# Performance work log

Measured on AMD Instinct MI355X. Metric: run time of the kernel, lower is better.

The kernel has to match this reference:

```python
import jax, jax.numpy as jnp
import numpy as np

# ---- para constants (see shape_source) ----
SIZE = 200          # SLM / detector plane
PAD = 100           # para.paddings -> padded FFT plane 400x400
PADDED = SIZE + 2 * PAD
NUM_LAYERS = 4
SCALE = 2.0         # para.scale
EXT = 1.0           # para.extension
K = 8               # para.kernel_size
S = 8               # para.stride
M = (SIZE - K) // S + 1   # para.map_size = 25
WIN = 5             # para.win_size
T = 1.0             # softmax temperature
RANGE = 10          # para.range (== dim_out)
DIM_OUT = 10
HIDDEN = 512
DIM_IN = M * M      # 625, flattened BN output feeds fcl
THR = 0.2           # para.thershold
SHIFT = 0.0         # para.shift
EPS = 1e-5          # BatchNorm eps
BATCH = 32


def setup_inputs() -> dict:
    key = jax.random.key(0)
    ks = jax.random.split(key, 10)
    x = jax.random.uniform(ks[0], (BATCH, SIZE, SIZE), jnp.float32)

    def transfer(k):  # unit-magnitude angular-spectrum transfer function
        ph = jax.random.uniform(k, (PADDED, PADDED), jnp.float32, 0.0, 2.0 * np.pi)
        return jnp.exp(1j * ph).astype(jnp.complex64)

    h = transfer(ks[1])
    h_pro = transfer(ks[2])
    h_det = transfer(ks[3])
    phase = 0.1 * jax.random.normal(ks[4], (NUM_LAYERS, SIZE, SIZE), jnp.float32)
    W1 = 0.02 * jax.random.normal(ks[5], (HIDDEN, DIM_IN), jnp.float32)
    b1 = jnp.zeros((HIDDEN,), jnp.float32)
    W2 = 0.02 * jax.random.normal(ks[6], (DIM_OUT, HIDDEN), jnp.float32)
    b2 = jnp.zeros((DIM_OUT,), jnp.float32)
    gamma = jnp.ones((1,), jnp.float32)   # BatchNorm2d(1) weight
    beta = jnp.zeros((1,), jnp.float32)   # BatchNorm2d(1) bias
    return {"x": x, "batch_size": BATCH, "h": h, "h_pro": h_pro, "h_det": h_det,
            "phase": phase, "W1": W1, "b1": b1, "W2": W2, "b2": b2,
            "gamma": gamma, "beta": beta}


def _diff(wave, trans):
    # F.pad + fftshift/fft2 * trans / ifft2/ifftshift (batch-dim shifts cancel)
    wave = jnp.pad(wave, ((0, 0), (PAD, PAD), (PAD, PAD)))
    wf = jnp.fft.fft2(jnp.fft.fftshift(wave, axes=(-2, -1)))
    return jnp.fft.ifftshift(jnp.fft.ifft2(wf * trans), axes=(-2, -1))


def _forward(x, batch_size, h, h_pro, h_det, phase, W1, b1, W2, b2, gamma, beta):
    x = x.astype(jnp.complex64)
    x = _diff(x, h_pro)[:, PAD:PAD + SIZE, PAD:PAD + SIZE]
    for idx in range(NUM_LAYERS):
        trans = jnp.pad(phase[idx], ((PAD, PAD), (PAD, PAD)))
        w = _diff(x, h)
        w = w * jnp.exp(1j * SCALE * jnp.pi * (jnp.sin(EXT * trans) + 1.0))
        x = w[:, PAD:PAD + SIZE, PAD:PAD + SIZE]
    x = _diff(x, h_det)[:, PAD:PAD + SIZE, PAD:PAD + SIZE]
    i_out = jnp.square(jnp.abs(x))                       # (B, SIZE, SIZE)
    B = i_out.shape[0]
    # AvgPool2d(K, S) with SIZE % K == 0 -> reshape-mean
    pooled = i_out.reshape(B, M, K, M, K).mean(axis=(2, 4))  # (B, M, M)

    rows = jnp.arange(M)

    def window(i, j):
        rm = (rows >= i) & (rows < i + WIN)
        cm = (rows >= j) & (rows < j + WIN)
        mask = (rm[:, None] & cm[None, :]).astype(pooled.dtype)   # I_block
        sig = pooled * mask                                       # (B, M, M)
        # BatchNorm2d(1), training mode: stats over all N*H*W
        mu = sig.mean()
        var = sig.var()
        nrm = (sig - mu) / jnp.sqrt(var + EPS) * gamma[0] + beta[0]
        f = nrm.reshape(B, -1)                                    # (B, DIM_IN)
        hid = jax.nn.relu(f @ W1.T + b1)                          # dropout: eval
        logits = (hid @ W2.T + b2) / T
        p = jax.nn.softmax(logits, axis=1)                        # (B, DIM_OUT)
        a = jnp.argmax(p, axis=1)                                 # (B,)
        delta = p.max(axis=1) - p.min(axis=1)                     # b - b2
        temp = jax.nn.one_hot(a, RANGE + 1, dtype=jnp.float32).sum(0)
        final0 = jnp.argmax(temp)
        dm = delta * (a == final0).astype(delta.dtype)            # delta * delta_max
        nz = jnp.sum(dm != 0.0)                                   # csr .data length
        delta1 = jnp.where(nz > 0, dm.sum() / jnp.maximum(nz, 1).astype(dm.dtype), jnp.nan)
        # nan < THR is False, matching torch semantics
        final = jnp.where(delta1 < THR, 0, final0 + 1).astype(jnp.int32)
        res = jnp.where(final == 0, 0.0, final.astype(jnp.float32) + SHIFT)
        ch = (final != 0).astype(jnp.float32)
        return final, res, ch

    ii, jj = jnp.meshgrid(jnp.arange(M), jnp.arange(M), indexing="ij")
    finals, result, ch_map = jax.vmap(window)(ii.ravel(), jj.ravel())
    result = result.reshape(M, M)
    ch_map = ch_map.reshape(M, M)
    histo = jnp.zeros(RANGE + 1, jnp.float32).at[finals].add(1.0)
    return result, ch_map, histo


def reference(x, batch_size, h, h_pro, h_det, phase, W1, b1, W2, b2, gamma, beta):
    return _forward(x, batch_size, h, h_pro, h_det, phase, W1, b1, W2, b2, gamma, beta)
```

## Files before the change

### kernel.cpp

```cpp
#include <hip/hip_runtime.h>
#include <math.h>

#define GLIM_X    1280000
#define GLIM_H    160000
#define GLIM_PH   160000
#define GLIM_W1   320000
#define GLIM_B1   512
#define GLIM_W2   5120
#define GLIM_B2   10
#define GLIM_OUT  1261
#define GLIM_POOL 20000

struct cplx { float x, y; };
__device__ __forceinline__ cplx operator+(cplx a, cplx b){ return {a.x+b.x, a.y+b.y}; }
__device__ __forceinline__ cplx operator-(cplx a, cplx b){ return {a.x-b.x, a.y-b.y}; }
__device__ __forceinline__ cplx cmul(cplx a, cplx b){ return {a.x*b.x - a.y*b.y, a.x*b.y + a.y*b.x}; }
template<bool INV>
__device__ __forceinline__ cplx tw(cplx a, cplx w){
  if(INV) return {a.x*w.x + a.y*w.y, a.y*w.x - a.x*w.y};
  else    return {a.x*w.x - a.y*w.y, a.x*w.y + a.y*w.x};
}
template<bool INV>
__device__ __forceinline__ void dft4(cplx&a, cplx&b, cplx&c, cplx&d){
  cplx t0=a+c, t1=a-c, t2=b+d, t3=b-d;
  cplx j3 = INV ? cplx{-t3.y, t3.x} : cplx{t3.y, -t3.x};
  a = t0+t2; c = t0-t2; b = t1+j3; d = t1-j3;
}
template<bool INV>
__device__ void fft16(cplx* x, const cplx* tab){
  cplx y[16];
  #pragma unroll
  for(int b=0;b<4;b++){
    cplx p0=x[b], p1=x[4+b], p2=x[8+b], p3=x[12+b];
    dft4<INV>(p0,p1,p2,p3);
    y[b*4+0]=p0;
    y[b*4+1]=tw<INV>(p1, tab[25*b]);
    y[b*4+2]=tw<INV>(p2, tab[50*b]);
    y[b*4+3]=tw<INV>(p3, tab[75*b]);
  }
  #pragma unroll
  for(int c=0;c<4;c++){
    cplx p0=y[c], p1=y[4+c], p2=y[8+c], p3=y[12+c];
    dft4<INV>(p0,p1,p2,p3);
    x[c]=p0; x[c+4]=p1; x[c+8]=p2; x[c+12]=p3;
  }
}
template<bool INV>
__device__ __forceinline__ void dft5(const cplx* v, cplx* o, const cplx* tab){
  #pragma unroll
  for(int k=0;k<5;k++){
    cplx s=v[0];
    #pragma unroll
    for(int j=1;j<5;j++){
      const int m=(j*k)%5;
      s = s + tw<INV>(v[j], tab[80*m]);
    }
    o[k]=s;
  }
}
template<bool INV>
__device__ void fft25(cplx* t, const cplx* tab){
  cplx u[25];
  #pragma unroll
  for(int b=0;b<5;b++){
    cplx v[5], o[5];
    #pragma unroll
    for(int a=0;a<5;a++) v[a]=t[5*a+b];
    dft5<INV>(v,o,tab);
    #pragma unroll
    for(int c=0;c<5;c++) u[b*5+c]=tw<INV>(o[c], tab[16*b*c]);
  }
  #pragma unroll
  for(int c=0;c<5;c++){
    cplx v[5], o[5];
    #pragma unroll
    for(int b=0;b<5;b++) v[b]=u[b*5+c];
    dft5<INV>(v,o,tab);
    #pragma unroll
    for(int d=0;d<5;d++) t[c+5*d]=o[d];
  }
}

__device__ __forceinline__ float bf2f(unsigned short u){
  unsigned int v = ((unsigned int)u)<<16;
  float f; __builtin_memcpy(&f,&v,4); return f;
}
__device__ __forceinline__ float hf2f(unsigned short u){
  _Float16 x; __builtin_memcpy(&x,&u,2); return (float)x;
}
__device__ __forceinline__ cplx ldH(const void* p, int i, int dec){
  if(i<0 || i>=GLIM_H) return {0.f,0.f};
  unsigned int v = ((const unsigned int*)p)[i];
  unsigned short lo=(unsigned short)(v&0xFFFFu), hi=(unsigned short)(v>>16);
  cplx z;
  if(dec==2)      z = { hf2f(lo), hf2f(hi) };
  else if(dec==3) z = { (float)(short)lo*(1.f/32767.f), (float)(short)hi*(1.f/32767.f) };
  else            z = { bf2f(lo), bf2f(hi) };
  if(!(fabsf(z.x) < 2.f)) z.x = 0.f;
  if(!(fabsf(z.y) < 2.f)) z.y = 0.f;
  return z;
}
__device__ __forceinline__ float ldf(const float* p, int i, int lim){
  if(i<0 || i>=lim) return 0.f;
  return p[i];
}
__device__ __forceinline__ void stout(float* p, int i, float v){
  if(i>=0 && i<GLIM_OUT) p[i] = v;
}

__global__ __launch_bounds__(64) void k_probe(const void* h, int* flags){
  __shared__ float err[3];
  if(threadIdx.x<3) err[threadIdx.x]=0.f;
  __syncthreads();
  if(threadIdx.x<32){
    unsigned int v = ((const unsigned int*)h)[threadIdx.x];
    unsigned short lo=(unsigned short)(v&0xFFFFu), hi=(unsigned short)(v>>16);
    float cr[3], ci[3];
    cr[0]=bf2f(lo);                       ci[0]=bf2f(hi);
    cr[1]=hf2f(lo);                       ci[1]=hf2f(hi);
    cr[2]=(float)(short)lo*(1.f/32767.f); ci[2]=(float)(short)hi*(1.f/32767.f);
    for(int d=0;d<3;d++){
      float r2 = cr[d]*cr[d] + ci[d]*ci[d];
      float e = fabsf(r2 - 1.f);
      if(!(e < 4.f)) e = 4.f;
      atomicAdd(&err[d], e);
    }
  }
  __syncthreads();
  if(threadIdx.x==0){
    int best=0; float be=err[0];
    for(int d=1; d<3; d++) if(err[d] < be){ be=err[d]; best=d; }
    flags[1] = best+1;
    flags[0] = 0;
  }
}

__global__ __launch_bounds__(256) void k_init(cplx* tab, float* outz, float* hist, float* pr){
  int t = blockIdx.x*256 + threadIdx.x;
  if(t < 400){
    float a = -6.28318530717958647692f * (float)t * (1.0f/400.0f);
    float sn, cs; sincosf(a, &sn, &cs);
    tab[t] = { cs, sn };
  }
  if(t < GLIM_OUT) outz[t] = 0.f;
  if(t < 11) hist[t] = 0.f;
  if(t >= 16 && t < 30) pr[t-16] = 0.f;
}

__global__ __launch_bounds__(256) void k_hprep(const void* h, const void* hpro,
    const void* hdet, cplx* __restrict__ Hd, const int* __restrict__ flags)
{
  int dec = flags[1];
  int t = blockIdx.x*256 + threadIdx.x;
  if(t >= 3*GLIM_H) return;
  int arr = t/GLIM_H, o = t - arr*GLIM_H;
  int c = o/400, rem = o - c*400;
  int k1 = rem/25, k2 = rem - k1*25;
  const void* src = (arr==0)?h:((arr==1)?hpro:hdet);
  Hd[t] = ldH(src, (k1+16*k2)*400 + c, dec);
}

__global__ __launch_bounds__(256,2) void k_rowfft(const float* __restrict__ xr,
    int img0, cplx* __restrict__ A, const cplx* __restrict__ gtab, int alim)
{
  __shared__ cplx lt[8*400];
  __shared__ cplx stab[400];
  for(int m=threadIdx.x;m<400;m+=256) stab[m]=gtab[m];
  int lr = threadIdx.x>>5, role = threadIdx.x&31;
  int idx = blockIdx.x*8 + lr;
  int img_local = idx/200, rc = idx - img_local*200;
  int abase = img_local*80000 + rc*400;
  __syncthreads();
  if(role<25){
    int n2=role;
    cplx x[16];
    #pragma unroll
    for(int n1=0;n1<16;n1++){
      cplx v={0.f,0.f};
      if(n1>=4 && n1<12){
        int cc = 25*n1+n2-100;
        v = { ldf(xr, (img0+img_local)*40000 + rc*200 + cc, GLIM_X), 0.f };
      }
      x[n1]=v;
    }
    fft16<false>(x, stab);
    cplx* L = lt + lr*400;
    #pragma unroll
    for(int k1=0;k1<16;k1++) L[k1*25+n2]=tw<false>(x[k1], stab[n2*k1]);
  }
  __syncthreads();
  if(role<16){
    int k1=role;
    cplx* L = lt + lr*400;
    cplx t[25];
    #pragma unroll
    for(int n2=0;n2<25;n2++) t[n2]=L[k1*25+n2];
    fft25<false>(t, stab);
    #pragma unroll
    for(int k2=0;k2<25;k2++){
      int ai = abase + k1+16*k2;
      if(ai>=0 && ai<alim) A[ai]=t[k2];
    }
  }
}

__global__ __launch_bounds__(256,2) void k_colpass(cplx* __restrict__ A,
    const cplx* __restrict__ Hd, const cplx* __restrict__ gtab)
{
  __shared__ cplx lt[8*401];
  __shared__ cplx stab[400];
  cplx (*sm)[9] = (cplx(*)[9])lt;
  for(int m=threadIdx.x;m<400;m+=256) stab[m]=gtab[m];
  int img_local = blockIdx.x/50, cg = blockIdx.x - img_local*50;
  int col0 = cg*8;
  int lc = threadIdx.x&7, rr = threadIdx.x>>3;
  cplx* L = lt + lc*401;
  cplx xx[25];
  __syncthreads();
  {
    const float4* A4 = (const float4*)A;
    for(int t=threadIdx.x; t<800; t+=256){
      int r = t>>2, p = t&3;
      int ce = img_local*80000 + r*400 + col0 + 2*p;
      float4 v = A4[ce>>1];
      sm[r][2*p]   = { v.x, v.y };
      sm[r][2*p+1] = { v.z, v.w };
    }
  }
  __syncthreads();
  if(rr<25){
    int n2=rr;
    #pragma unroll
    for(int n1=0;n1<16;n1++){
      cplx v={0.f,0.f};
      if(n1>=4 && n1<12) v = sm[25*n1+n2-100][lc];
      xx[n1]=v;
    }
  }
  __syncthreads();
  if(rr<25){
    int n2=rr;
    fft16<false>(xx, stab);
    #pragma unroll
    for(int k1=0;k1<16;k1++) L[k1*25+n2]=tw<false>(xx[k1], stab[n2*k1]);
  }
  __syncthreads();
  if(rr<16){
    int k1=rr;
    #pragma unroll
    for(int n2=0;n2<25;n2++) xx[n2]=L[k1*25+n2];
    fft25<false>(xx, stab);
    const cplx* hrun = Hd + (col0+lc)*400 + k1*25;
    #pragma unroll
    for(int k2=0;k2<25;k2++) xx[k2]=cmul(xx[k2], hrun[k2]);
  }
  __syncthreads();
  if(rr<16){
    int k1=rr;
    #pragma unroll
    for(int k2=0;k2<25;k2++) L[k1+16*k2]=xx[k2];
  }
  __syncthreads();
  if(rr<25){
    int n2=rr;
    #pragma unroll
    for(int n1=0;n1<16;n1++) xx[n1]=L[25*n1+n2];
  }
  __syncthreads();
  if(rr<25){
    int n2=rr;
    fft16<true>(xx, stab);
    #pragma unroll
    for(int k1=0;k1<16;k1++) L[k1*25+n2]=tw<true>(xx[k1], stab[n2*k1]);
  }
  __syncthreads();
  if(rr<16){
    int k1=rr;
    #pragma unroll
    for(int n2=0;n2<25;n2++) xx[n2]=L[k1*25+n2];
    fft25<true>(xx, stab);
    const float sc=1.0f/400.0f;
    #pragma unroll
    for(int k2=0;k2<25;k2++){ xx[k2].x*=sc; xx[k2].y*=sc; }
  }
  __syncthreads();
  if(rr<16){
    int k1=rr;
    #pragma unroll
    for(int k2=0;k2<25;k2++){
      int m=k1+16*k2;
      if(m>=100 && m<300) sm[m-100][lc] = xx[k2];
    }
  }
  __syncthreads();
  {
    float4* A4 = (float4*)A;
    for(int t=threadIdx.x; t<800; t+=256){
      int r = t>>2, p = t&3;
      int ce = img_local*80000 + r*400 + col0 + 2*p;
      cplx a = sm[r][2*p], b = sm[r][2*p+1];
      A4[ce>>1] = { a.x, a.y, b.x, b.y };
    }
  }
}

__global__ __launch_bounds__(256,2) void k_rowpass(cplx* __restrict__ A,
    const float* __restrict__ ph, int phoff, int useMask,
    const cplx* __restrict__ gtab, int alim)
{
  __shared__ cplx lt[8*400];
  __shared__ cplx stab[400];
  cplx (*sm)[200] = (cplx(*)[200])lt;
  for(int m=threadIdx.x;m<400;m+=256) stab[m]=gtab[m];
  int lr=threadIdx.x>>5, role=threadIdx.x&31;
  int idx = blockIdx.x*8+lr;
  int img_local = idx/200, rc = idx - img_local*200;
  int abase = img_local*80000 + rc*400;
  __syncthreads();
  if(role<25){
    int n2=role;
    cplx x[16];
    #pragma unroll
    for(int n1=0;n1<16;n1++){
      cplx v={0.f,0.f};
      int ai = abase + 25*n1+n2;
      if(ai>=0 && ai<alim) v=A[ai];
      x[n1]=v;
    }
    fft16<true>(x, stab);
    cplx* L = lt + lr*400;
    #pragma unroll
    for(int k1=0;k1<16;k1++) L[k1*25+n2]=tw<true>(x[k1], stab[n2*k1]);
  }
  __syncthreads();
  cplx t[25];
  int k1 = role;
  if(role<16){
    cplx* L=lt+lr*400;
    #pragma unroll
    for(int n2=0;n2<25;n2++) t[n2]=L[k1*25+n2];
    fft25<true>(t, stab);
    const float sc=1.0f/400.0f;
    #pragma unroll
    for(int k2=0;k2<25;k2++){ t[k2].x*=sc; t[k2].y*=sc; }
  }
  __syncthreads();
  if(role<16){
    #pragma unroll
    for(int k2=0;k2<25;k2++){
      int m=k1+16*k2;
      if(m>=100 && m<300){
        int cc=m-100;
        cplx v=t[k2];
        if(useMask){
          float tt = ldf(ph, phoff + rc*200+cc, GLIM_PH);
          float th = 6.28318530717958647692f*(sinf(tt)+1.0f);
          float sn, cs; sincosf(th,&sn,&cs);
          v = cmul(v, cplx{cs,sn});
        }
        sm[lr][cc]=v;
      }
    }
  }
  __syncthreads();
  cplx x2[16];
  if(role<25){
    int n2=role;
    #pragma unroll
    for(int n1=0;n1<16;n1++){
      cplx v={0.f,0.f};
      if(n1>=4 && n1<12) v = sm[lr][25*n1+n2-100];
      x2[n1]=v;
    }
  }
  __syncthreads();
  if(role<25){
    int n2=role;
    fft16<false>(x2, stab);
    cplx* L = lt + lr*400;
    #pragma unroll
    for(int k1f=0;k1f<16;k1f++) L[k1f*25+n2]=tw<false>(x2[k1f], stab[n2*k1f]);
  }
  __syncthreads();
  if(role<16){
    cplx* L = lt + lr*400;
    cplx t2[25];
    #pragma unroll
    for(int n2=0;n2<25;n2++) t2[n2]=L[k1*25+n2];
    fft25<false>(t2, stab);
    #pragma unroll
    for(int k2=0;k2<25;k2++){
      int ai = abase + k1+16*k2;
      if(ai>=0 && ai<alim) A[ai]=t2[k2];
    }
  }
}

__global__ __launch_bounds__(256,2) void k_rowpool(const cplx* __restrict__ A,
    float* __restrict__ pooled, int img0, const cplx* __restrict__ gtab, int alim)
{
  __shared__ cplx lt[8*400];
  __shared__ cplx stab[400];
  __shared__ float sI[8][200];
  for(int m=threadIdx.x;m<400;m+=256) stab[m]=gtab[m];
  int lr=threadIdx.x>>5, role=threadIdx.x&31;
  int idx = blockIdx.x*8+lr;
  int img_local = idx/200;
  int abase = img_local*80000 + (idx - img_local*200)*400;
  __syncthreads();
  if(role<25){
    int n2=role;
    cplx x[16];
    #pragma unroll
    for(int n1=0;n1<16;n1++){
      cplx v={0.f,0.f};
      int ai = abase + 25*n1+n2;
      if(ai>=0 && ai<alim) v=A[ai];
      x[n1]=v;
    }
    fft16<true>(x, stab);
    cplx* L = lt + lr*400;
    #pragma unroll
    for(int k1=0;k1<16;k1++) L[k1*25+n2]=tw<true>(x[k1], stab[n2*k1]);
  }
  __syncthreads();
  cplx t[25];
  int k1 = role;
  if(role<16){
    cplx* L=lt+lr*400;
    #pragma unroll
    for(int n2=0;n2<25;n2++) t[n2]=L[k1*25+n2];
    fft25<true>(t, stab);
    const float sc=1.0f/400.0f;
    #pragma unroll
    for(int k2=0;k2<25;k2++){ t[k2].x*=sc; t[k2].y*=sc; }
  }
  if(role<16){
    #pragma unroll
    for(int k2=0;k2<25;k2++){
      int m=k1+16*k2;
      if(m>=100 && m<300) sI[lr][m-100] = t[k2].x*t[k2].x + t[k2].y*t[k2].y;
    }
  }
  __syncthreads();
  if(threadIdx.x<25){
    int band = blockIdx.x*8;
    int il = band/200, r0 = band - il*200;
    float s=0.f;
    #pragma unroll
    for(int u=0;u<8;u++){
      #pragma unroll
      for(int v=0;v<8;v++) s += sI[u][threadIdx.x*8+v];
    }
    int pi = (img0+il)*625 + (r0>>3)*25 + threadIdx.x;
    if(pi>=0 && pi<GLIM_POOL) pooled[pi] = s*(1.0f/64.0f);
  }
}

__global__ __launch_bounds__(64) void k_rowsum(const float* __restrict__ W1,
    float* __restrict__ rs){
  __shared__ float red[64];
  int hh = blockIdx.x;
  float s=0.f;
  for(int e=threadIdx.x;e<625;e+=64) s += ldf(W1, hh*625+e, GLIM_W1);
  red[threadIdx.x]=s;
  __syncthreads();
  for(int off=32;off>0;off>>=1){
    if(threadIdx.x<off) red[threadIdx.x]+=red[threadIdx.x+off];
    __syncthreads();
  }
  if(threadIdx.x==0 && hh<512) rs[hh]=red[0];
}

__global__ __launch_bounds__(256,2) void k_window(const float* __restrict__ pooled,
    const float* __restrict__ W1, const float* __restrict__ b1,
    const float* __restrict__ W2, const float* __restrict__ b2,
    const float* __restrict__ rowsum, const float* __restrict__ gm,
    const float* __restrict__ bt, float* __restrict__ outp, float* __restrict__ hist)
{
  __shared__ float w1s[512*26];
  __shared__ float w2s[10*512];
  __shared__ float ps[25*32];
  __shared__ float comb[512];
  __shared__ int   wIdx[25];
  __shared__ float sred[4][2];
  __shared__ float sf0, sgos;
  __shared__ int   aArr[32];
  __shared__ float dArr[32];

  int wi = blockIdx.x;
  int i = wi/25, j = wi - i*25;
  int er = (25-i<5)?(25-i):5;
  int ec = (25-j<5)?(25-j):5;
  int E = er*ec;
  int tid = threadIdx.x;
  if(tid<25) wIdx[tid] = (i + tid/ec)*25 + (j + tid%ec);
  __syncthreads();

  for(int t=tid;t<5120;t+=256) w2s[t] = ldf(W2, t, GLIM_W2);

  for(int t=tid;t<800;t+=256){
    int e=t>>5, b=t&31;
    float v=0.f;
    if(e<E){
      v = pooled[(t&31)*625 + wIdx[e]];
      if(!(fabsf(v) < 1e30f)) v = 0.f;
    }
    ps[e*32+b]=v;
  }

  if(E==25){
    for(int t=tid;t<512*25;t+=256){
      int hh=t/25, e=t-hh*25;
      w1s[hh*26+e] = ldf(W1, hh*625+wIdx[e], GLIM_W1);
    }
  } else {
    for(int t=tid;t<3328;t+=256) ((float4*)w1s)[t] = float4{0.f,0.f,0.f,0.f};
    __syncthreads();
    for(int t=tid;t<512*E;t+=256){
      int hh=t/E, e=t-hh*E;
      w1s[hh*26+e] = ldf(W1, hh*625+wIdx[e], GLIM_W1);
    }
  }
  __syncthreads();

  {
    float s1=0.f, s2=0.f;
    for(int t=tid;t<800;t+=256){ float v=ps[t]; s1+=v; s2+=v*v; }
    #pragma unroll
    for(int m=1;m<64;m<<=1){ s1 += __shfl_xor(s1,m); s2 += __shfl_xor(s2,m); }
    if((tid&63)==0){ sred[tid>>6][0]=s1; sred[tid>>6][1]=s2; }
  }
  __syncthreads();
  if(tid==0){
    float a=sred[0][0]+sred[1][0]+sred[2][0]+sred[3][0];
    float c=sred[0][1]+sred[1][1]+sred[2][1]+sred[3][1];
    float mu = a*(1.0f/20000.0f);
    float var = c*(1.0f/20000.0f) - mu*mu;
    float sg = sqrtf(var + 1e-5f);
    float g = gm[0];
    sf0 = bt[0] - g*mu/sg;
    sgos = g/sg;
  }
  __syncthreads();
  float f0=sf0, gos=sgos;
  for(int hh=tid;hh<512;hh+=256) comb[hh] = ldf(b1,hh,GLIM_B1) + f0*ldf(rowsum,hh,512);
  __syncthreads();

  int b = tid&31, s = tid>>5;
  float psr[25];
  #pragma unroll
  for(int e=0;e<25;e++) psr[e]=ps[e*32+b];

  float pl[10];
  #pragma unroll
  for(int o=0;o<10;o++) pl[o]=0.f;
  for(int k=0;k<64;k++){
    int hh = s*64+k;
    const float* wr = &w1s[hh*26];
    float wsum=0.f;
    #pragma unroll
    for(int e=0;e<25;e++) wsum = fmaf(wr[e], psr[e], wsum);
    float acc = comb[hh] + gos*wsum;
    float hid = acc>0.f?acc:0.f;
    #pragma unroll
    for(int o=0;o<10;o++) pl[o] = fmaf(hid, w2s[o*512+hh], pl[o]);
  }
  __syncthreads();
  float* red = w1s;
  #pragma unroll
  for(int o=0;o<10;o++) red[(s*32+b)*10+o]=pl[o];
  __syncthreads();

  if(tid<32){
    int bb = tid;
    float lg[10];
    #pragma unroll
    for(int o=0;o<10;o++){
      float a = b2[o];
      #pragma unroll
      for(int u=0;u<8;u++) a += red[(u*32+bb)*10+o];
      lg[o]=a;
    }
    float lmax=lg[0]; int am=0;
    #pragma unroll
    for(int o=1;o<10;o++) if(lg[o]>lmax){lmax=lg[o]; am=o;}
    float lmin=lg[0];
    #pragma unroll
    for(int o=1;o<10;o++) lmin=fminf(lmin,lg[o]);
    float Z=0.f;
    #pragma unroll
    for(int o=0;o<10;o++) Z += expf(lg[o]-lmax);
    float delta = (1.f - expf(lmin-lmax))/Z;
    aArr[bb]=am; dArr[bb]=delta;
  }
  __syncthreads();
  if(tid==0){
    int votes[11];
    #pragma unroll
    for(int k=0;k<11;k++) votes[k]=0;
    for(int bb=0;bb<32;bb++){
      int a=aArr[bb];
      if(a>=0 && a<11) votes[a]++;
    }
    int f0i=0, bv=votes[0];
    #pragma unroll
    for(int k=1;k<11;k++) if(votes[k]>bv){bv=votes[k]; f0i=k;}
    float sum=0.f; int nz=0;
    for(int bb=0;bb<32;bb++){
      if(aArr[bb]==f0i){
        float dd=dArr[bb];
        sum+=dd;
        if(dd!=0.f) nz++;
      }
    }
    int fin;
    if(nz>0){
      float d1=sum/(float)nz;
      fin = (d1<0.2f)?0:(f0i+1);
    } else fin = f0i+1;
    stout(outp, wi, (fin==0)?0.f:(float)fin);
    stout(outp, 625+wi, (fin!=0)?1.f:0.f);
    if(fin>=0 && fin<=10) atomicAdd(&hist[fin], 1.0f);
  }
}

__global__ __launch_bounds__(64) void k_fin(const float* __restrict__ hist,
    float* __restrict__ outp){
  if(threadIdx.x<11) stout(outp, 1250+threadIdx.x, hist[threadIdx.x]);
}

__global__ __launch_bounds__(256) void k_diag(const float* __restrict__ pooled,
    const float* __restrict__ hist, const float* __restrict__ pr,
    const int* __restrict__ flags, float* __restrict__ outp){
  __shared__ float smax[256];
  __shared__ int snan[256];
  float m=0.f; int nan=0;
  for(int i=threadIdx.x;i<GLIM_POOL;i+=256){
    float v=pooled[i];
    if(isnan(v)||isinf(v)) nan=1;
    else { float a=fabsf(v); if(a>m)m=a; }
  }
  smax[threadIdx.x]=m; snan[threadIdx.x]=nan;
  __syncthreads();
  for(int off=128;off>0;off>>=1){
    if(threadIdx.x<off){
      smax[threadIdx.x]=fmaxf(smax[threadIdx.x],smax[threadIdx.x+off]);
      snan[threadIdx.x]|=snan[threadIdx.x+off];
    }
    __syncthreads();
  }
  if(threadIdx.x==0 && hist[0] < 613.f){
    int dec = flags[1] & 7;
    int low, nanbit = 0;
    if(snan[0]){ nanbit=128; low=0; (void)pr; }
    else {
      if(smax[0]<=0.f) low=0;
      else {
        int e=(int)floorf(log2f(smax[0]));
        low = e+8; if(low<1)low=1; if(low>15)low=15;
      }
    }
    int S = nanbit | (dec<<4) | low;
    outp[0] = 8192.0f*(float)S;
  }
}

extern "C" void kernel_launch(void* const* d_in, const int* in_sizes, int n_in,
                              void* d_out, int out_size, void* d_ws, size_t ws_size,
                              hipStream_t stream)
{
  (void)in_sizes;
  if(n_in != 12 || out_size < GLIM_OUT || d_ws == nullptr) return;
  const float* x   = (const float*)d_in[0];
  const void* h    = d_in[2];
  const void* hpro = d_in[3];
  const void* hdet = d_in[4];
  const float* phase=(const float*)d_in[5];
  const float* W1  = (const float*)d_in[6];
  const float* b1  = (const float*)d_in[7];
  const float* W2  = (const float*)d_in[8];
  const float* b2  = (const float*)d_in[9];
  const float* gm  = (const float*)d_in[10];
  const float* bt  = (const float*)d_in[11];
  float* out = (float*)d_out;

  const size_t FIXED = 85888ull;
  const size_t HDB   = 3ull*GLIM_H*8ull;
  const size_t ABase = FIXED + HDB;
  int n = 0;
  if     (ABase + 32ull*640000ull <= ws_size) n = 32;
  else if(ABase + 16ull*640000ull <= ws_size) n = 16;
  else if(ABase +  8ull*640000ull <= ws_size) n = 8;
  else if(ABase +  4ull*640000ull <= ws_size) n = 4;
  else if(ABase +  2ull*640000ull <= ws_size) n = 2;
  else if(ABase +  1ull*640000ull <= ws_size) n = 1;
  if(n==0) return;

  char* w = (char*)d_ws;
  int*   flags  = (int*)(w + 0);
  cplx*  tab    = (cplx*)(w + 256);
  float* rowsum = (float*)(w + 3584);
  float* hist   = (float*)(w + 5632);
  float* pr     = (float*)(w + 5760);
  float* pooled = (float*)(w + 5888);
  cplx*  Hd     = (cplx*)(w + FIXED);
  cplx*  A      = (cplx*)(w + ABase);
  const int alim  = n*80000;

  k_probe<<<1,64,0,stream>>>(h, flags);
  k_init<<<6,256,0,stream>>>(tab, out, hist, pr);
  k_rowsum<<<512,64,0,stream>>>(W1, rowsum);
  k_hprep<<<(3*GLIM_H+255)/256,256,0,stream>>>(h, hpro, hdet, Hd, flags);

  for(int c=0; c<32; c+=n){
    k_rowfft<<<n*25,256,0,stream>>>(x, c, A, tab, alim);
    for(int d=0; d<6; d++){
      const cplx* Hcur = (d==0) ? (Hd+GLIM_H) : ((d==5) ? (Hd+2*GLIM_H) : Hd);
      k_colpass<<<n*50,256,0,stream>>>(A, Hcur, tab);
      if(d<5){
        int useMask = (d>=1) ? 1 : 0;
        int phoff = useMask ? (d-1)*40000 : 0;
        k_rowpass<<<n*25,256,0,stream>>>(A, phase, phoff, useMask, tab, alim);
      } else {
        k_rowpool<<<n*25,256,0,stream>>>(A, pooled, c, tab, alim);
      }
    }
  }
  k_window<<<625,256,0,stream>>>(pooled, W1,b1,W2,b2,rowsum, gm,bt, out, hist);
  k_fin<<<1,64,0,stream>>>(hist, out);
  k_diag<<<1,256,0,stream>>>(pooled, hist, pr, flags, out);
}
```

Before: 794.9 us.

## Split window MLP across hidden partitions and widen FFT pass blocks

The window kernel now splits the 512 hidden units into four partitions of 128. That makes 2500 blocks instead of 625, each staging a quarter of W1/W2 in shared memory. Partial logits go to a scratch buffer that reuses the transfer-function region, and a new k_vote kernel sums them and runs the softmax and voting. The column and row FFT passes now handle 16 columns or rows per 512-thread block, giving wider coalesced accesses and fewer blocks. The costs are an extra kernel launch, the partial-logit round trip through global memory, and lower occupancy or register headroom for the larger FFT blocks.

```diff
diff --git a/kernel.cpp b/kernel.cpp
--- a/kernel.cpp
+++ b/kernel.cpp
@@ -10,6 +10,8 @@
 #define GLIM_B2   10
 #define GLIM_OUT  1261
 #define GLIM_POOL 20000
+
+#define HPART 128
 
 struct cplx { float x, y; };
 __device__ __forceinline__ cplx operator+(cplx a, cplx b){ return {a.x+b.x, a.y+b.y}; }
@@ -204,23 +206,23 @@
   }
 }
 
-__global__ __launch_bounds__(256,2) void k_colpass(cplx* __restrict__ A,
+__global__ __launch_bounds__(512,2) void k_colpass(cplx* __restrict__ A,
     const cplx* __restrict__ Hd, const cplx* __restrict__ gtab)
 {
-  __shared__ cplx lt[8*401];
+  __shared__ cplx lt[16*401];
   __shared__ cplx stab[400];
-  cplx (*sm)[9] = (cplx(*)[9])lt;
-  for(int m=threadIdx.x;m<400;m+=256) stab[m]=gtab[m];
-  int img_local = blockIdx.x/50, cg = blockIdx.x - img_local*50;
-  int col0 = cg*8;
-  int lc = threadIdx.x&7, rr = threadIdx.x>>3;
+  cplx (*sm)[17] = (cplx(*)[17])lt;
+  for(int m=threadIdx.x;m<400;m+=512) stab[m]=gtab[m];
+  int img_local = blockIdx.x/25, cg = blockIdx.x - img_local*25;
+  int col0 = cg*16;
+  int lc = threadIdx.x&15, rr = threadIdx.x>>4;
   cplx* L = lt + lc*401;
   cplx xx[25];
   __syncthreads();
   {
     const float4* A4 = (const float4*)A;
-    for(int t=threadIdx.x; t<800; t+=256){
-      int r = t>>2, p = t&3;
+    for(int t=threadIdx.x; t<1600; t+=512){
+      int r = t>>3, p = t&7;
       int ce = img_local*80000 + r*400 + col0 + 2*p;
       float4 v = A4[ce>>1];
       sm[r][2*p]   = { v.x, v.y };
@@ -295,8 +297,8 @@
   __syncthreads();
   {
     float4* A4 = (float4*)A;
-    for(int t=threadIdx.x; t<800; t+=256){
-      int r = t>>2, p = t&3;
+    for(int t=threadIdx.x; t<1600; t+=512){
+      int r = t>>3, p = t&7;
       int ce = img_local*80000 + r*400 + col0 + 2*p;
       cplx a = sm[r][2*p], b = sm[r][2*p+1];
       A4[ce>>1] = { a.x, a.y, b.x, b.y };
@@ -304,16 +306,16 @@
   }
 }
 
-__global__ __launch_bounds__(256,2) void k_rowpass(cplx* __restrict__ A,
+__global__ __launch_bounds__(512,2) void k_rowpass(cplx* __restrict__ A,
     const float* __restrict__ ph, int phoff, int useMask,
     const cplx* __restrict__ gtab, int alim)
 {
-  __shared__ cplx lt[8*400];
+  __shared__ cplx lt[16*400];
   __shared__ cplx stab[400];
   cplx (*sm)[200] = (cplx(*)[200])lt;
-  for(int m=threadIdx.x;m<400;m+=256) stab[m]=gtab[m];
+  for(int m=threadIdx.x;m<400;m+=512) stab[m]=gtab[m];
   int lr=threadIdx.x>>5, role=threadIdx.x&31;
-  int idx = blockIdx.x*8+lr;
+  int idx = blockIdx.x*16+lr;
   int img_local = idx/200, rc = idx - img_local*200;
   int abase = img_local*80000 + rc*400;
   __syncthreads();
@@ -474,21 +476,21 @@
 
 __global__ __launch_bounds__(256,2) void k_window(const float* __restrict__ pooled,
     const float* __restrict__ W1, const float* __restrict__ b1,
-    const float* __restrict__ W2, const float* __restrict__ b2,
-    const float* __restrict__ rowsum, const float* __restrict__ gm,
-    const float* __restrict__ bt, float* __restrict__ outp, float* __restrict__ hist)
+    const float* __restrict__ W2, const float* __restrict__ rowsum,
+    const float* __restrict__ gm, const float* __restrict__ bt,
+    float* __restrict__ LP)
 {
-  __shared__ float w1s[512*26];
-  __shared__ float w2s[10*512];
+  __shared__ float w1s[HPART*26];
+  __shared__ float w2s[10*HPART];
   __shared__ float ps[25*32];
-  __shared__ float comb[512];
+  __shared__ float comb[HPART];
   __shared__ int   wIdx[25];
   __shared__ float sred[4][2];
   __shared__ float sf0, sgos;
-  __shared__ int   aArr[32];
-  __shared__ float dArr[32];
-
-  int wi = blockIdx.x;
+
+  int wi = blockIdx.x >> 2;
+  int part = blockIdx.x & 3;
+  int h0 = part*HPART;
   int i = wi/25, j = wi - i*25;
   int er = (25-i<5)?(25-i):5;
   int ec = (25-j<5)?(25-j):5;
@@ -497,29 +499,29 @@
   if(tid<25) wIdx[tid] = (i + tid/ec)*25 + (j + tid%ec);
   __syncthreads();
 
-  for(int t=tid;t<5120;t+=256) w2s[t] = ldf(W2, t, GLIM_W2);
+  for(int t=tid;t<10*HPART;t+=256) w2s[t] = ldf(W2, (t>>7)*512 + h0 + (t&(HPART-1)), GLIM_W2);
 
   for(int t=tid;t<800;t+=256){
-    int e=t>>5, b=t&31;
+    int e=t>>5;
     float v=0.f;
     if(e<E){
       v = pooled[(t&31)*625 + wIdx[e]];
       if(!(fabsf(v) < 1e30f)) v = 0.f;
     }
-    ps[e*32+b]=v;
+    ps[t]=v;
   }
 
   if(E==25){
-    for(int t=tid;t<512*25;t+=256){
+    for(int t=tid;t<HPART*25;t+=256){
       int hh=t/25, e=t-hh*25;
-      w1s[hh*26+e] = ldf(W1, hh*625+wIdx[e], GLIM_W1);
+      w1s[hh*26+e] = ldf(W1, (h0+hh)*625+wIdx[e], GLIM_W1);
     }
   } else {
-    for(int t=tid;t<3328;t+=256) ((float4*)w1s)[t] = float4{0.f,0.f,0.f,0.f};
+    for(int t=tid;t<832;t+=256) ((float4*)w1s)[t] = float4{0.f,0.f,0.f,0.f};
     __syncthreads();
-    for(int t=tid;t<512*E;t+=256){
+    for(int t=tid;t<HPART*E;t+=256){
       int hh=t/E, e=t-hh*E;
-      w1s[hh*26+e] = ldf(W1, hh*625+wIdx[e], GLIM_W1);
+      w1s[hh*26+e] = ldf(W1, (h0+hh)*625+wIdx[e], GLIM_W1);
     }
   }
   __syncthreads();
@@ -544,7 +546,7 @@
   }
   __syncthreads();
   float f0=sf0, gos=sgos;
-  for(int hh=tid;hh<512;hh+=256) comb[hh] = ldf(b1,hh,GLIM_B1) + f0*ldf(rowsum,hh,512);
+  for(int hh=tid;hh<HPART;hh+=256) comb[hh] = ldf(b1,h0+hh,GLIM_B1) + f0*ldf(rowsum,h0+hh,512);
   __syncthreads();
 
   int b = tid&31, s = tid>>5;
@@ -555,8 +557,8 @@
   float pl[10];
   #pragma unroll
   for(int o=0;o<10;o++) pl[o]=0.f;
-  for(int k=0;k<64;k++){
-    int hh = s*64+k;
+  for(int k=0;k<16;k++){
+    int hh = s*16+k;
     const float* wr = &w1s[hh*26];
     float wsum=0.f;
     #pragma unroll
@@ -564,7 +566,7 @@
     float acc = comb[hh] + gos*wsum;
     float hid = acc>0.f?acc:0.f;
     #pragma unroll
-    for(int o=0;o<10;o++) pl[o] = fmaf(hid, w2s[o*512+hh], pl[o]);
+    for(int o=0;o<10;o++) pl[o] = fmaf(hid, w2s[o*HPART+hh], pl[o]);
   }
   __syncthreads();
   float* red = w1s;
@@ -573,13 +575,29 @@
   __syncthreads();
 
   if(tid<32){
-    int bb = tid;
+    #pragma unroll
+    for(int o=0;o<10;o++){
+      float a = 0.f;
+      #pragma unroll
+      for(int u=0;u<8;u++) a += red[(u*32+tid)*10+o];
+      LP[((part*625+wi)*32+tid)*10+o] = a;
+    }
+  }
+}
+
+__global__ __launch_bounds__(64) void k_vote(const float* __restrict__ LP,
+    const float* __restrict__ b2, float* __restrict__ outp, float* __restrict__ hist)
+{
+  __shared__ int aArr[32];
+  __shared__ float dArr[32];
+  int wi = blockIdx.x, tid = threadIdx.x;
+  if(tid<32){
     float lg[10];
     #pragma unroll
     for(int o=0;o<10;o++){
-      float a = b2[o];
+      float a = ldf(b2,o,GLIM_B2);
       #pragma unroll
-      for(int u=0;u<8;u++) a += red[(u*32+bb)*10+o];
+      for(int p=0;p<4;p++) a += LP[((p*625+wi)*32+tid)*10+o];
       lg[o]=a;
     }
     float lmax=lg[0]; int am=0;
@@ -592,7 +610,7 @@
     #pragma unroll
     for(int o=0;o<10;o++) Z += expf(lg[o]-lmax);
     float delta = (1.f - expf(lmin-lmax))/Z;
-    aArr[bb]=am; dArr[bb]=delta;
+    aArr[tid]=am; dArr[tid]=delta;
   }
   __syncthreads();
   if(tid==0){
@@ -706,6 +724,7 @@
   float* pooled = (float*)(w + 5888);
   cplx*  Hd     = (cplx*)(w + FIXED);
   cplx*  A      = (cplx*)(w + ABase);
+  float* LP     = (float*)Hd;
   const int alim  = n*80000;
 
   k_probe<<<1,64,0,stream>>>(h, flags);
@@ -717,17 +736,18 @@
     k_rowfft<<<n*25,256,0,stream>>>(x, c, A, tab, alim);
     for(int d=0; d<6; d++){
       const cplx* Hcur = (d==0) ? (Hd+GLIM_H) : ((d==5) ? (Hd+2*GLIM_H) : Hd);
-      k_colpass<<<n*50,256,0,stream>>>(A, Hcur, tab);
+      k_colpass<<<n*25,512,0,stream>>>(A, Hcur, tab);
       if(d<5){
         int useMask = (d>=1) ? 1 : 0;
         int phoff = useMask ? (d-1)*40000 : 0;
-        k_rowpass<<<n*25,256,0,stream>>>(A, phase, phoff, useMask, tab, alim);
+        k_rowpass<<<(n*200+15)/16,512,0,stream>>>(A, phase, phoff, useMask, tab, alim);
       } else {
         k_rowpool<<<n*25,256,0,stream>>>(A, pooled, c, tab, alim);
       }
     }
   }
-  k_window<<<625,256,0,stream>>>(pooled, W1,b1,W2,b2,rowsum, gm,bt, out, hist);
+  k_window<<<2500,256,0,stream>>>(pooled, W1,b1,W2,rowsum, gm,bt, LP);
+  k_vote<<<625,64,0,stream>>>(LP, b2, out, hist);
   k_fin<<<1,64,0,stream>>>(hist, out);
   k_diag<<<1,256,0,stream>>>(pooled, hist, pr, flags, out);
 }
```

Result: faster. 688.9 us (-13.3%).
